# Kernel tuning notes

Measured on AMD Instinct MI355X. Metric: run time of the kernel, lower is better.

Reference implementation:

```python
import jax, jax.numpy as jnp
import numpy as np

B, S, H = 4, 4096, 2048
E = 64          # num_routed_experts
TOP_K = 8
TEMP = 1.0      # router_temperature


def setup_inputs() -> dict:
    key = jax.random.key(0)
    k1, k2 = jax.random.split(key)
    hidden_states = jax.random.normal(k1, (B, S, H), dtype=jnp.float32)
    # nn.Linear weight: [out_features, in_features] = [E, H]
    gate_w = jax.random.normal(k2, (E, H), dtype=jnp.float32) * (1.0 / np.sqrt(H))
    return {"hidden_states": hidden_states, "gate_w": gate_w}


def reference(hidden_states, gate_w):
    # Gate projection + temperature scaling: [B,S,H] @ [H,E] -> [B,S,E]
    router_logits = jnp.einsum("bsh,eh->bse", hidden_states, gate_w) / TEMP
    # Top-k over experts
    routing_weights, selected_experts = jax.lax.top_k(router_logits, TOP_K)
    # Softmax over the top-k slots in fp32, cast back to input dtype
    routing_weights = jax.nn.softmax(routing_weights.astype(jnp.float32), axis=-1).astype(hidden_states.dtype)
    return router_logits, routing_weights, selected_experts
```

## Files before the change

kernel.cpp:

```cpp
#include <hip/hip_runtime.h>
#include <math.h>

#define HH 2048
#define EE 64
#define TOPK 8
#define NT 16384
#define MT 64
#define KC 16
#define KQR 512
#define NCH 32
#define LS 68

typedef __attribute__((ext_vector_type(8)))  short short8;
typedef __attribute__((ext_vector_type(16))) float f32x16;

static __device__ __forceinline__ void cvt3(const float4& a, const float4& b,
                                            short8& h, short8& m, short8& l)
{
    const float v[8] = {a.x, a.y, a.z, a.w, b.x, b.y, b.z, b.w};
#pragma unroll
    for (int i = 0; i < 8; ++i) {
        const unsigned int u = __float_as_uint(v[i]);
        h[i] = (short)(u >> 16);
        const float r1 = v[i] - __uint_as_float(u & 0xffff0000u);
        const unsigned int u1 = __float_as_uint(r1);
        m[i] = (short)(u1 >> 16);
        const float r2 = r1 - __uint_as_float(u1 & 0xffff0000u);
        const unsigned int u2 = __float_as_uint(r2);
        l[i] = (short)((u2 + 0x7fffu + ((u2 >> 16) & 1u)) >> 16);
    }
}

static __device__ __forceinline__ int swz_unit(int p, int e, int cb)
{
    const int v   = (p * 64 + e) * 2 + cb;
    const int low = (((e & 3) * 2 + cb) ^ ((e >> 2) & 7));
    return (v & ~7) | low;
}

__global__ __launch_bounds__(256) void wsplit(
    const float* __restrict__ w, short* __restrict__ wsw)
{
    const int e = blockIdx.x;
    const int o = threadIdx.x;
    const int k = o * 8;
    const float4 a = *(const float4*)(w + (size_t)e * HH + k);
    const float4 b = *(const float4*)(w + (size_t)e * HH + k + 4);
    short8 h, m, l;
    cvt3(a, b, h, m, l);

    const int kq = k >> 9;
    const int c  = (k & 511) >> 4;
    const int cb = (k >> 3) & 1;
    const size_t base = ((size_t)c * 4 + kq) * 384;
    *(short8*)(wsw + (base + swz_unit(0, e, cb)) * 8) = h;
    *(short8*)(wsw + (base + swz_unit(1, e, cb)) * 8) = m;
    *(short8*)(wsw + (base + swz_unit(2, e, cb)) * 8) = l;
}

__global__ __launch_bounds__(512, 2) void router_fused(
    const float* __restrict__ x,
    const short* __restrict__ wsw,
    float* __restrict__ out_logits,
    float* __restrict__ out_wts,
    float* __restrict__ out_idx)
{
    __shared__ __align__(16) char smem_raw[49152];
    short* ldsw = (short*)smem_raw;
    float* slog = (float*)smem_raw;

    const int t    = threadIdx.x;
    const int wv   = t >> 6;
    const int lane = t & 63;
    const int g    = wv >> 2;
    const int kq   = wv & 3;
    const int l5   = lane >> 5;
    const int lr   = lane & 31;
    const int tok0 = blockIdx.x * MT;

    const float* xp = x + (size_t)(tok0 + g * 32 + lr) * HH + kq * KQR + l5 * 8;

    f32x16 accM0 = {0}, accM1 = {0};
    f32x16 accS0 = {0}, accS1 = {0};

    auto stage = [&](int c, int buf) {
        const short* src = wsw + ((size_t)c * 1536 + t) * 8;
        short* dst = ldsw + ((size_t)buf * 1536 + t) * 8;
#pragma unroll
        for (int i = 0; i < 3; ++i)
            *(short8*)(dst + (size_t)i * 512 * 8) =
                *(const short8*)(src + (size_t)i * 512 * 8);
    };

    auto compute = [&](const float4& xa, const float4& xb, int buf) {
        short8 xh, xm, xl;
        cvt3(xa, xb, xh, xm, xl);
        const short* base = ldsw + ((size_t)buf * 1536 + kq * 384) * 8;
#pragma unroll
        for (int eb = 0; eb < 2; ++eb) {
            const int e = eb * 32 + lr;
            const short8 bh = *(const short8*)(base + swz_unit(0, e, l5) * 8);
            const short8 bm = *(const short8*)(base + swz_unit(1, e, l5) * 8);
            const short8 bl = *(const short8*)(base + swz_unit(2, e, l5) * 8);
            f32x16& AM = eb ? accM1 : accM0;
            f32x16& AS = eb ? accS1 : accS0;
            AM = __builtin_amdgcn_mfma_f32_32x32x16_bf16(xh, bh, AM, 0, 0, 0);
            AS = __builtin_amdgcn_mfma_f32_32x32x16_bf16(xh, bm, AS, 0, 0, 0);
            AS = __builtin_amdgcn_mfma_f32_32x32x16_bf16(xm, bh, AS, 0, 0, 0);
            AS = __builtin_amdgcn_mfma_f32_32x32x16_bf16(xh, bl, AS, 0, 0, 0);
            AS = __builtin_amdgcn_mfma_f32_32x32x16_bf16(xl, bh, AS, 0, 0, 0);
            AS = __builtin_amdgcn_mfma_f32_32x32x16_bf16(xm, bm, AS, 0, 0, 0);
        }
    };

    stage(0, 0);
    float4 xa0 = *(const float4*)(xp);
    float4 xa1 = *(const float4*)(xp + 4);
    float4 xb0 = *(const float4*)(xp + KC);
    float4 xb1 = *(const float4*)(xp + KC + 4);
    __syncthreads();

#pragma unroll 1
    for (int c = 0; c < NCH; c += 2) {
        stage(c + 1, 1);
        compute(xa0, xa1, 0);
        if (c + 2 < NCH) {
            xa0 = *(const float4*)(xp + (c + 2) * KC);
            xa1 = *(const float4*)(xp + (c + 2) * KC + 4);
        }
        __syncthreads();

        if (c + 2 < NCH) stage(c + 2, 0);
        compute(xb0, xb1, 1);
        if (c + 3 < NCH) {
            xb0 = *(const float4*)(xp + (c + 3) * KC);
            xb1 = *(const float4*)(xp + (c + 3) * KC + 4);
        }
        __syncthreads();
    }

#pragma unroll 1
    for (int q = 0; q < 4; ++q) {
        if (kq == q) {
#pragma unroll
            for (int eb = 0; eb < 2; ++eb) {
                const f32x16& AM = eb ? accM1 : accM0;
                const f32x16& AS = eb ? accS1 : accS0;
                const int col = eb * 32 + lr;
#pragma unroll
                for (int r = 0; r < 16; ++r) {
                    const int row = g * 32 + (r & 3) + 8 * (r >> 2) + 4 * l5;
                    const float val = AM[r] + AS[r];
                    if (q == 0) slog[row * LS + col] = val;
                    else        slog[row * LS + col] += val;
                }
            }
        }
        __syncthreads();
    }

    {
        const int row = t >> 3;
        const int c8  = (t & 7) * 8;
        const float4 o0 = *(const float4*)&slog[row * LS + c8];
        const float4 o1 = *(const float4*)&slog[row * LS + c8 + 4];
        float* dst = out_logits + (size_t)(tok0 + row) * EE + c8;
        *(float4*)dst       = o0;
        *(float4*)(dst + 4) = o1;
    }

    if (t < MT) {
        float tv[TOPK];
        int   ti[TOPK];
#pragma unroll
        for (int q = 0; q < TOPK; ++q) { tv[q] = -INFINITY; ti[q] = 0; }

        for (int e = 0; e < EE; ++e) {
            const float val = slog[t * LS + e];
            if (val > tv[TOPK - 1]) {
                tv[TOPK - 1] = val;
                ti[TOPK - 1] = e;
#pragma unroll
                for (int q = TOPK - 1; q > 0; --q) {
                    if (tv[q] > tv[q - 1]) {
                        float fv = tv[q]; tv[q] = tv[q - 1]; tv[q - 1] = fv;
                        int   fi = ti[q]; ti[q] = ti[q - 1]; ti[q - 1] = fi;
                    }
                }
            }
        }

        const float m = tv[0];
        float ew[TOPK];
        float sum = 0.f;
#pragma unroll
        for (int q = 0; q < TOPK; ++q) { ew[q] = expf(tv[q] - m); sum += ew[q]; }
        const float inv = 1.f / sum;

        const size_t tok = (size_t)(tok0 + t);
        float4 w0, w1, i0, i1;
        w0.x = ew[0] * inv; w0.y = ew[1] * inv; w0.z = ew[2] * inv; w0.w = ew[3] * inv;
        w1.x = ew[4] * inv; w1.y = ew[5] * inv; w1.z = ew[6] * inv; w1.w = ew[7] * inv;
        i0.x = (float)ti[0]; i0.y = (float)ti[1]; i0.z = (float)ti[2]; i0.w = (float)ti[3];
        i1.x = (float)ti[4]; i1.y = (float)ti[5]; i1.z = (float)ti[6]; i1.w = (float)ti[7];
        *(float4*)(out_wts + tok * TOPK)     = w0;
        *(float4*)(out_wts + tok * TOPK + 4) = w1;
        *(float4*)(out_idx + tok * TOPK)     = i0;
        *(float4*)(out_idx + tok * TOPK + 4) = i1;
    }
}

extern "C" void kernel_launch(void* const* d_in, const int* in_sizes, int n_in,
                              void* d_out, int out_size, void* d_ws, size_t ws_size,
                              hipStream_t stream) {
    const float* x = (const float*)d_in[0];
    const float* w = (const float*)d_in[1];
    float* out        = (float*)d_out;
    float* out_logits = out;
    float* out_wts    = out + (size_t)NT * EE;
    float* out_idx    = out_wts + (size_t)NT * TOPK;
    short* wsw = (short*)d_ws;

    hipLaunchKernelGGL(wsplit, dim3(EE), dim3(256), 0, stream, w, wsw);
    hipLaunchKernelGGL(router_fused, dim3(NT / MT), dim3(512), 0, stream,
                       x, wsw, out_logits, out_wts, out_idx);
}
```

Measured before the change: 224.2 us.

## Drop weight pre-split kernel and LDS staging; load fp32 weights directly per wave

Removes the separate kernel that split the gate weights into swizzled bf16 hi/mid/lo planes, and removes the double-buffered LDS staging with its per-chunk barriers. Each wave now loads x and both 32-expert halves of the fp32 weights straight from global memory into registers, with a four-chunk software prefetch, and does the three-way bf16 split in registers. The tile shrinks to 32 tokens and 256 threads per block, which doubles the number of blocks. The goal is to cut launch overhead and synchronisation stalls, at the cost of re-reading the full weight matrix from L2 in every block and repeating the weight split in every wave.

After: 231.9 us. 3.5% more time.

```diff
diff --git a/kernel.cpp b/kernel.cpp
--- a/kernel.cpp
+++ b/kernel.cpp
@@ -5,7 +5,7 @@
 #define EE 64
 #define TOPK 8
 #define NT 16384
-#define MT 64
+#define MT 32
 #define KC 16
 #define KQR 512
 #define NCH 32
@@ -31,112 +31,76 @@
     }
 }
 
-static __device__ __forceinline__ int swz_unit(int p, int e, int cb)
-{
-    const int v   = (p * 64 + e) * 2 + cb;
-    const int low = (((e & 3) * 2 + cb) ^ ((e >> 2) & 7));
-    return (v & ~7) | low;
-}
-
-__global__ __launch_bounds__(256) void wsplit(
-    const float* __restrict__ w, short* __restrict__ wsw)
-{
-    const int e = blockIdx.x;
-    const int o = threadIdx.x;
-    const int k = o * 8;
-    const float4 a = *(const float4*)(w + (size_t)e * HH + k);
-    const float4 b = *(const float4*)(w + (size_t)e * HH + k + 4);
-    short8 h, m, l;
-    cvt3(a, b, h, m, l);
-
-    const int kq = k >> 9;
-    const int c  = (k & 511) >> 4;
-    const int cb = (k >> 3) & 1;
-    const size_t base = ((size_t)c * 4 + kq) * 384;
-    *(short8*)(wsw + (base + swz_unit(0, e, cb)) * 8) = h;
-    *(short8*)(wsw + (base + swz_unit(1, e, cb)) * 8) = m;
-    *(short8*)(wsw + (base + swz_unit(2, e, cb)) * 8) = l;
-}
-
-__global__ __launch_bounds__(512, 2) void router_fused(
+__global__ __launch_bounds__(256, 2) void router_fused(
     const float* __restrict__ x,
-    const short* __restrict__ wsw,
+    const float* __restrict__ w,
     float* __restrict__ out_logits,
     float* __restrict__ out_wts,
     float* __restrict__ out_idx)
 {
-    __shared__ __align__(16) char smem_raw[49152];
-    short* ldsw = (short*)smem_raw;
-    float* slog = (float*)smem_raw;
+    __shared__ float slog[MT * LS];
 
     const int t    = threadIdx.x;
     const int wv   = t >> 6;
     const int lane = t & 63;
-    const int g    = wv >> 2;
-    const int kq   = wv & 3;
+    const int kq   = wv;
     const int l5   = lane >> 5;
     const int lr   = lane & 31;
     const int tok0 = blockIdx.x * MT;
 
-    const float* xp = x + (size_t)(tok0 + g * 32 + lr) * HH + kq * KQR + l5 * 8;
+    const float* xp  = x + (size_t)(tok0 + lr) * HH + kq * KQR + l5 * 8;
+    const float* wp0 = w + (size_t)(lr)      * HH + kq * KQR + l5 * 8;
+    const float* wp1 = w + (size_t)(32 + lr) * HH + kq * KQR + l5 * 8;
 
     f32x16 accM0 = {0}, accM1 = {0};
     f32x16 accS0 = {0}, accS1 = {0};
 
-    auto stage = [&](int c, int buf) {
-        const short* src = wsw + ((size_t)c * 1536 + t) * 8;
-        short* dst = ldsw + ((size_t)buf * 1536 + t) * 8;
-#pragma unroll
-        for (int i = 0; i < 3; ++i)
-            *(short8*)(dst + (size_t)i * 512 * 8) =
-                *(const short8*)(src + (size_t)i * 512 * 8);
+    struct Chunk { float4 x0, x1, a0, a1, b0, b1; };
+    Chunk S0, S1, S2, S3;
+
+    auto load = [&](Chunk& s, int c) {
+        const int o = c * KC;
+        s.x0 = *(const float4*)(xp  + o);
+        s.x1 = *(const float4*)(xp  + o + 4);
+        s.a0 = *(const float4*)(wp0 + o);
+        s.a1 = *(const float4*)(wp0 + o + 4);
+        s.b0 = *(const float4*)(wp1 + o);
+        s.b1 = *(const float4*)(wp1 + o + 4);
     };
 
-    auto compute = [&](const float4& xa, const float4& xb, int buf) {
+    auto compute = [&](const Chunk& s) {
         short8 xh, xm, xl;
-        cvt3(xa, xb, xh, xm, xl);
-        const short* base = ldsw + ((size_t)buf * 1536 + kq * 384) * 8;
-#pragma unroll
-        for (int eb = 0; eb < 2; ++eb) {
-            const int e = eb * 32 + lr;
-            const short8 bh = *(const short8*)(base + swz_unit(0, e, l5) * 8);
-            const short8 bm = *(const short8*)(base + swz_unit(1, e, l5) * 8);
-            const short8 bl = *(const short8*)(base + swz_unit(2, e, l5) * 8);
-            f32x16& AM = eb ? accM1 : accM0;
-            f32x16& AS = eb ? accS1 : accS0;
-            AM = __builtin_amdgcn_mfma_f32_32x32x16_bf16(xh, bh, AM, 0, 0, 0);
-            AS = __builtin_amdgcn_mfma_f32_32x32x16_bf16(xh, bm, AS, 0, 0, 0);
-            AS = __builtin_amdgcn_mfma_f32_32x32x16_bf16(xm, bh, AS, 0, 0, 0);
-            AS = __builtin_amdgcn_mfma_f32_32x32x16_bf16(xh, bl, AS, 0, 0, 0);
-            AS = __builtin_amdgcn_mfma_f32_32x32x16_bf16(xl, bh, AS, 0, 0, 0);
-            AS = __builtin_amdgcn_mfma_f32_32x32x16_bf16(xm, bm, AS, 0, 0, 0);
+        cvt3(s.x0, s.x1, xh, xm, xl);
+        {
+            short8 bh, bm, bl;
+            cvt3(s.a0, s.a1, bh, bm, bl);
+            accM0 = __builtin_amdgcn_mfma_f32_32x32x16_bf16(xh, bh, accM0, 0, 0, 0);
+            accS0 = __builtin_amdgcn_mfma_f32_32x32x16_bf16(xh, bm, accS0, 0, 0, 0);
+            accS0 = __builtin_amdgcn_mfma_f32_32x32x16_bf16(xm, bh, accS0, 0, 0, 0);
+            accS0 = __builtin_amdgcn_mfma_f32_32x32x16_bf16(xh, bl, accS0, 0, 0, 0);
+            accS0 = __builtin_amdgcn_mfma_f32_32x32x16_bf16(xl, bh, accS0, 0, 0, 0);
+            accS0 = __builtin_amdgcn_mfma_f32_32x32x16_bf16(xm, bm, accS0, 0, 0, 0);
+        }
+        {
+            short8 bh, bm, bl;
+            cvt3(s.b0, s.b1, bh, bm, bl);
+            accM1 = __builtin_amdgcn_mfma_f32_32x32x16_bf16(xh, bh, accM1, 0, 0, 0);
+            accS1 = __builtin_amdgcn_mfma_f32_32x32x16_bf16(xh, bm, accS1, 0, 0, 0);
+            accS1 = __builtin_amdgcn_mfma_f32_32x32x16_bf16(xm, bh, accS1, 0, 0, 0);
+            accS1 = __builtin_amdgcn_mfma_f32_32x32x16_bf16(xh, bl, accS1, 0, 0, 0);
+            accS1 = __builtin_amdgcn_mfma_f32_32x32x16_bf16(xl, bh, accS1, 0, 0, 0);
+            accS1 = __builtin_amdgcn_mfma_f32_32x32x16_bf16(xm, bm, accS1, 0, 0, 0);
         }
     };
 
-    stage(0, 0);
-    float4 xa0 = *(const float4*)(xp);
-    float4 xa1 = *(const float4*)(xp + 4);
-    float4 xb0 = *(const float4*)(xp + KC);
-    float4 xb1 = *(const float4*)(xp + KC + 4);
-    __syncthreads();
+    load(S0, 0); load(S1, 1); load(S2, 2); load(S3, 3);
 
 #pragma unroll 1
-    for (int c = 0; c < NCH; c += 2) {
-        stage(c + 1, 1);
-        compute(xa0, xa1, 0);
-        if (c + 2 < NCH) {
-            xa0 = *(const float4*)(xp + (c + 2) * KC);
-            xa1 = *(const float4*)(xp + (c + 2) * KC + 4);
-        }
-        __syncthreads();
-
-        if (c + 2 < NCH) stage(c + 2, 0);
-        compute(xb0, xb1, 1);
-        if (c + 3 < NCH) {
-            xb0 = *(const float4*)(xp + (c + 3) * KC);
-            xb1 = *(const float4*)(xp + (c + 3) * KC + 4);
-        }
-        __syncthreads();
+    for (int c = 0; c < NCH; c += 4) {
+        compute(S0); if (c + 4 < NCH) load(S0, c + 4);
+        compute(S1); if (c + 5 < NCH) load(S1, c + 5);
+        compute(S2); if (c + 6 < NCH) load(S2, c + 6);
+        compute(S3); if (c + 7 < NCH) load(S3, c + 7);
     }
 
 #pragma unroll 1
@@ -149,7 +113,7 @@
                 const int col = eb * 32 + lr;
 #pragma unroll
                 for (int r = 0; r < 16; ++r) {
-                    const int row = g * 32 + (r & 3) + 8 * (r >> 2) + 4 * l5;
+                    const int row = (r & 3) + 8 * (r >> 2) + 4 * l5;
                     const float val = AM[r] + AS[r];
                     if (q == 0) slog[row * LS + col] = val;
                     else        slog[row * LS + col] += val;
@@ -219,9 +183,7 @@
     float* out_logits = out;
     float* out_wts    = out + (size_t)NT * EE;
     float* out_idx    = out_wts + (size_t)NT * TOPK;
-    short* wsw = (short*)d_ws;
 
-    hipLaunchKernelGGL(wsplit, dim3(EE), dim3(256), 0, stream, w, wsw);
-    hipLaunchKernelGGL(router_fused, dim3(NT / MT), dim3(512), 0, stream,
-                       x, wsw, out_logits, out_wts, out_idx);
+    hipLaunchKernelGGL(router_fused, dim3(NT / MT), dim3(256), 0, stream,
+                       x, w, out_logits, out_wts, out_idx);
 }
```
